# Optimization experiments

Measured on AMD Instinct MI355X. Metric: run time of the kernel, lower is better.

The kernel has to match this reference:

```python
import jax, jax.numpy as jnp
import numpy as np
from jax import lax

SEQ, BATCH, IN, H, L = 2048, 64, 512, 3, 4


def setup_inputs() -> dict:
    key = jax.random.key(0)
    ks = jax.random.split(key, 10)
    s_in = 1.0 / np.sqrt(H)  # torch GRU init scale: U(-1/sqrt(H), 1/sqrt(H))
    u = lambda k, shape: jax.random.uniform(k, shape, jnp.float32, -s_in, s_in)
    return {
        "x": jax.random.normal(ks[0], (SEQ, BATCH, IN), jnp.float32),
        "hxs": jnp.zeros((L, BATCH, H), jnp.float32),
        "w_ih0": u(ks[1], (3 * H, IN)),
        "w_hh0": u(ks[2], (3 * H, H)),
        "b_ih0": u(ks[3], (3 * H,)),
        "b_hh0": u(ks[4], (3 * H,)),
        "w_ih_rest": u(ks[5], (L - 1, 3 * H, H)),
        "w_hh_rest": u(ks[6], (L - 1, 3 * H, H)),
        "b_ih_rest": u(ks[7], (L - 1, 3 * H)),
        "b_hh_rest": u(ks[8], (L - 1, 3 * H)),
    }


def _gru_layer(x_seq, h0, w_ih, w_hh, b_ih, b_hh):
    # Precompute input projections for the whole sequence: (T, B, 3H)
    gx = jnp.einsum("tbi,gi->tbg", x_seq, w_ih) + b_ih

    def step(h, gx_t):
        gh = h @ w_hh.T + b_hh  # (B, 3H)
        rx, zx, nx = jnp.split(gx_t, 3, axis=-1)
        rh, zh, nh = jnp.split(gh, 3, axis=-1)
        r = jax.nn.sigmoid(rx + rh)
        z = jax.nn.sigmoid(zx + zh)
        n = jnp.tanh(nx + r * nh)
        h_new = (1.0 - z) * n + z * h
        return h_new, h_new

    h_last, ys = lax.scan(step, h0, gx)
    return ys, h_last


def reference(x, hxs, w_ih0, w_hh0, b_ih0, b_hh0, w_ih_rest, w_hh_rest, b_ih_rest, b_hh_rest):
    out, h = _gru_layer(x, hxs[0], w_ih0, w_hh0, b_ih0, b_hh0)
    h_finals = [h]
    for l in range(w_ih_rest.shape[0]):  # small fixed layer count
        out, h = _gru_layer(out, hxs[l + 1], w_ih_rest[l], w_hh_rest[l], b_ih_rest[l], b_hh_rest[l])
        h_finals.append(h)
    return out, jnp.stack(h_finals)  # (T, B, H), (L, B, H)
```

## Files before the change

### kernel.cpp

```cpp
#include <hip/hip_runtime.h>
#include <hip/hip_bf16.h>

#define T_SEQ 2048
#define CHUNK 16
#define NCHUNK 129
#define L2E  1.44269504088896340736f
#define L2E2 2.88539008177792681472f

typedef float vf2 __attribute__((ext_vector_type(2)));

template<int CTRL>
__device__ __forceinline__ float dppmov(float v) {
    return __int_as_float(__builtin_amdgcn_update_dpp(
        0, __float_as_int(v), CTRL, 0xF, 0xF, true));
}
template<int CTRL>
__device__ __forceinline__ float dppadd(float v) { return v + dppmov<CTRL>(v); }
__device__ __forceinline__ float swzadd16(float v) {
    return v + __int_as_float(__builtin_amdgcn_ds_swizzle(__float_as_int(v), 0x401F));
}
__device__ __forceinline__ float frcp(float x) { return __builtin_amdgcn_rcpf(x); }
__device__ __forceinline__ float ex2(float x)  { return __builtin_amdgcn_exp2f(x); }
__device__ __forceinline__ vf2 pkfma(vf2 a, float b, vf2 c) {
    vf2 bb = { b, b };
    return __builtin_elementwise_fma(a, bb, c);
}

#define RING_BARRIER() asm volatile("s_waitcnt lgkmcnt(0)\ns_barrier" ::: "memory")

__global__ __launch_bounds__(256) void gx0_kernel(
    const float* __restrict__ x, const float* __restrict__ w,
    const float* __restrict__ bias, float* __restrict__ gx0)
{
    const int lane = threadIdx.x & 63;
    const int gw   = (blockIdx.x * 256 + threadIdx.x) >> 6;

    float4 wA[9], wB[9];
#pragma unroll
    for (int g = 0; g < 9; ++g) {
        const float s = (g < 6) ? L2E : -L2E2;
        float4 a = *(const float4*)&w[g * 512 + lane * 4];
        float4 b = *(const float4*)&w[g * 512 + 256 + lane * 4];
        wA[g] = make_float4(a.x * s, a.y * s, a.z * s, a.w * s);
        wB[g] = make_float4(b.x * s, b.y * s, b.z * s, b.w * s);
    }
    const float bval = (lane < 9) ? bias[lane] * ((lane < 6) ? L2E : -L2E2) : 0.f;

    size_t row0 = (size_t)gw * 16;
    const float4* xp = (const float4*)(x + row0 * 512);
    float4 xa = xp[lane];
    float4 xb = xp[64 + lane];

#pragma unroll 1
    for (int i = 0; i < 16; ++i) {
        float4 na = xa, nb = xb;
        if (i < 15) {
            na = xp[(i + 1) * 128 + lane];
            nb = xp[(i + 1) * 128 + 64 + lane];
        }
        float r[9];
#pragma unroll
        for (int g = 0; g < 9; ++g) {
            float s = xa.x * wA[g].x;
            s = fmaf(xa.y, wA[g].y, s);
            s = fmaf(xa.z, wA[g].z, s);
            s = fmaf(xa.w, wA[g].w, s);
            s = fmaf(xb.x, wB[g].x, s);
            s = fmaf(xb.y, wB[g].y, s);
            s = fmaf(xb.z, wB[g].z, s);
            s = fmaf(xb.w, wB[g].w, s);
            s = dppadd<0xB1>(s);
            s = dppadd<0x4E>(s);
            s = dppadd<0x124>(s);
            s = dppadd<0x128>(s);
            s = swzadd16(s);
            s += __shfl_xor(s, 32, 64);
            r[g] = s;
        }
        float o = r[0];
#pragma unroll
        for (int g = 1; g < 9; ++g) o = (lane == g) ? r[g] : o;
        if (lane < 9) gx0[(row0 + i) * 9 + lane] = fminf(fmaxf(o + bval, -50.f), 50.f);
        xa = na; xb = nb;
    }
}

__global__ __launch_bounds__(128) void gru_scan(
    const float* __restrict__ gx0,
    const float* __restrict__ hxs,
    const float* __restrict__ w_hh0, const float* __restrict__ b_hh0,
    const float* __restrict__ w_ih_rest, const float* __restrict__ w_hh_rest,
    const float* __restrict__ b_ih_rest, const float* __restrict__ b_hh_rest,
    float* __restrict__ out)
{
    __shared__ float gxf[3 * CHUNK * 3 * 64];
    __shared__ float ring[2][CHUNK][64];
    const int tid  = threadIdx.x;
    const int lane = tid & 63;

    if (tid < 64) {
        __builtin_amdgcn_s_setprio(1);
        const int grp = lane >> 4;
        const int r_  = lane & 15;
        const int l   = r_ >> 2;
        const int j   = r_ & 3;
        const bool jok = (j < 3);
        const bool is0 = (l == 0);
        const int  b   = blockIdx.x * 4 + grp;
        const int  row0 = jok ? j : 0;

        int lx[4];
#pragma unroll
        for (int q = 0; q < 4; ++q) lx[q] = lane ^ (q << 2);

        vf2 wi01[3], wh01[3], bh01;
        float wi2[3], wh2[3], bh2;
        {
            float wi[3][3], wh[3][3], bh[3];
            const float sc[3] = {L2E, L2E, -L2E2};
#pragma unroll
            for (int m = 0; m < 3; ++m) {
                const int row = m * 3 + row0;
                if (l == 0) {
                    bh[m] = b_hh0[row] * sc[m];
#pragma unroll
                    for (int k = 0; k < 3; ++k) { wi[m][k] = 0.f; wh[m][k] = w_hh0[row * 3 + k] * sc[m]; }
                } else {
                    float bb = b_hh_rest[(l - 1) * 9 + row];
                    if (m < 2) bb += b_ih_rest[(l - 1) * 9 + row];
                    bh[m] = bb * sc[m];
#pragma unroll
                    for (int k = 0; k < 3; ++k) {
                        wi[m][k] = w_ih_rest[((l - 1) * 9 + row) * 3 + k] * sc[m];
                        wh[m][k] = w_hh_rest[((l - 1) * 9 + row) * 3 + k] * sc[m];
                    }
                }
            }
#pragma unroll
            for (int k = 0; k < 3; ++k) {
                wi01[k] = (vf2){wi[0][k], wi[1][k]};
                wh01[k] = (vf2){wh[0][k], wh[1][k]};
                wi2[k] = wi[2][k]; wh2[k] = wh[2][k];
            }
            bh01 = (vf2){bh[0], bh[1]};
            bh2  = bh[2];
        }
        const float bi2 = is0 ? 0.f : b_ih_rest[(l - 1) * 9 + 6 + row0] * (-L2E2);

        if (!(is0 && jok)) {
            const float cm[3] = {0.f, 0.f, bi2};
#pragma unroll
            for (int f = 0; f < 3; ++f)
                for (int st = 0; st < CHUNK; ++st)
#pragma unroll
                    for (int m = 0; m < 3; ++m)
                        gxf[((f * CHUNK + st) * 3 + m) * 64 + lx[(st * 3 + m) & 3]] = cm[m];
        }
        float h = jok ? hxs[(l * 64 + b) * 3 + j] : 0.f;

        RING_BARRIER();

        float gp[4][3];
#define PREF(SL, BUF, ST)                                                           \
        do {                                                                        \
            const float* _r = gxf + ((BUF) * CHUNK + (ST)) * 192;                   \
            gp[SL][0] = _r[lx[((ST) * 3 + 0) & 3]];                                 \
            gp[SL][1] = _r[64 + lx[((ST) * 3 + 1) & 3]];                            \
            gp[SL][2] = _r[128 + lx[((ST) * 3 + 2) & 3]];                           \
        } while (0)

#pragma unroll
        for (int k = 0; k < 4; ++k) PREF(k, 0, k);

        int bufc = 0;

#define GSTEP(P, MODE, TT)                                                          \
        do {                                                                        \
            float c0 = gp[(P) & 3][0], c1 = gp[(P) & 3][1], c2 = gp[(P) & 3][2];    \
            if ((P) < CHUNK - 4) PREF((P) & 3, bufc, (P) + 4);                      \
            else                 PREF((P) & 3, bufn, (P) - (CHUNK - 4));            \
            float hv0 = dppmov<0x00>(h);                                            \
            float hv1 = dppmov<0x55>(h);                                            \
            float hv2 = dppmov<0xAA>(h);                                            \
            float xv0 = dppmov<0x114>(hv0);                                         \
            float xv1 = dppmov<0x114>(hv1);                                         \
            float xv2 = dppmov<0x114>(hv2);                                         \
            vf2 t1 = pkfma(wh01[0], hv0, bh01);                                     \
            vf2 t2 = pkfma(wh01[1], hv1, (vf2){c0, c1});                            \
            t1 = pkfma(wh01[2], hv2, t1);                                           \
            t2 = pkfma(wi01[0], xv0, t2);                                           \
            t1 = pkfma(wi01[1], xv1, t1);                                           \
            t2 = pkfma(wi01[2], xv2, t2);                                           \
            vf2 arz = t1 + t2;                                                      \
            float ghn = fmaf(wh2[0], hv0, fmaf(wh2[1], hv1, fmaf(wh2[2], hv2, bh2))); \
            float gxn = fmaf(wi2[0], xv0, fmaf(wi2[1], xv1, fmaf(wi2[2], xv2, c2))); \
            float er = ex2(-arz.x);                                                 \
            float ez = ex2(-arz.y);                                                 \
            float rr = frcp(1.0f + er);                                             \
            float argn = fmaf(rr, ghn, gxn);                                        \
            float en = ex2(argn);                                                   \
            float hm = h - ez;                                                      \
            float hp = h + ez;                                                      \
            float N  = fmaf(en, hm, hp);                                            \
            float enp1 = en + 1.0f;                                                 \
            float D  = fmaf(enp1, ez, enp1);                                        \
            float hn = N * frcp(D);                                                 \
            if (MODE == 0)      h = ((TT) >= 0)    ? hn : h;                        \
            else if (MODE == 2) h = ((TT) < T_SEQ) ? hn : h;                        \
            else                h = hn;                                             \
            ring[CB][(P)][lane] = hn;                                               \
        } while (0)

        {
            const int bufn = 1; const int CB = 0;
#pragma unroll
            for (int p = 0; p < 4; ++p)  GSTEP(p, 0, p - l);
#pragma unroll
            for (int p = 4; p < 16; ++p) GSTEP(p, 1, 0);
            RING_BARRIER();
            bufc = 1;
        }
#pragma unroll 1
        for (int c = 1; c < 128; ++c) {
            const int bufn = (bufc == 2) ? 0 : bufc + 1;
            const int CB = c & 1;
#pragma unroll
            for (int p = 0; p < 16; ++p) GSTEP(p, 1, 0);
            RING_BARRIER();
            bufc = bufn;
        }
        {
            const int bufn = (bufc == 2) ? 0 : bufc + 1;
            const int CB = 0;
#pragma unroll
            for (int p = 0; p < 4; ++p) GSTEP(p, 2, 2048 + p - l);
            RING_BARRIER();
        }
#undef GSTEP
#undef PREF
        if (jok) out[(size_t)T_SEQ * 192 + (l * 64 + b) * 3 + j] = h;
    } else {
        const int blk = blockIdx.x;

#define FILL(F, T0)                                                                 \
        do {                                                                        \
            _Pragma("unroll")                                                       \
            for (int k = 0; k < 9; ++k) {                                           \
                int i   = k * 64 + lane;                                            \
                int st  = i / 36;                                                   \
                int rem = i - st * 36;                                              \
                int m   = rem / 12;                                                 \
                int pos = rem - m * 12;                                             \
                int bl  = pos / 3;                                                  \
                int jj  = pos - bl * 3;                                             \
                float val = gx0[(size_t)((T0) + st) * 576 + (blk * 4 + bl) * 9 + m * 3 + jj]; \
                int slot = (bl * 16 + jj) ^ ((((st * 3 + m) & 3)) << 2);            \
                gxf[(((F) * CHUNK + st) * 3 + m) * 64 + slot] = val;                \
            }                                                                       \
        } while (0)

#define DRAIN(CC)                                                                   \
        do {                                                                        \
            _Pragma("unroll")                                                       \
            for (int k = 0; k < 3; ++k) {                                           \
                int i  = k * 64 + lane;                                             \
                int p  = i / 12;                                                    \
                int q  = i - p * 12;                                                \
                int g2 = q / 3;                                                     \
                int jj = q - g2 * 3;                                                \
                int t  = (CC) * CHUNK + p - 3;                                      \
                float val = ring[(CC) & 1][p][g2 * 16 + 12 + jj];                   \
                if (t >= 0 && t < T_SEQ)                                            \
                    out[(size_t)t * 192 + (blk * 4 + g2) * 3 + jj] = val;           \
            }                                                                       \
        } while (0)

        FILL(0, 0);
        FILL(1, CHUNK);
        RING_BARRIER();

#pragma unroll 1
        for (int c = 0; c < NCHUNK; ++c) {
            const int f = c + 2;
            if (f <= 127) FILL(f % 3, f * CHUNK);
            if (c >= 1)   DRAIN(c - 1);
            RING_BARRIER();
        }
        DRAIN(NCHUNK - 1);
#undef FILL
#undef DRAIN
    }
}

extern "C" void kernel_launch(void* const* d_in, const int* in_sizes, int n_in,
                              void* d_out, int out_size, void* d_ws, size_t ws_size,
                              hipStream_t stream) {
    const float* x         = (const float*)d_in[0];
    const float* hxs       = (const float*)d_in[1];
    const float* w_ih0     = (const float*)d_in[2];
    const float* w_hh0     = (const float*)d_in[3];
    const float* b_ih0     = (const float*)d_in[4];
    const float* b_hh0     = (const float*)d_in[5];
    const float* w_ih_rest = (const float*)d_in[6];
    const float* w_hh_rest = (const float*)d_in[7];
    const float* b_ih_rest = (const float*)d_in[8];
    const float* b_hh_rest = (const float*)d_in[9];
    float* out = (float*)d_out;
    float* gx0 = (float*)d_ws;

    hipLaunchKernelGGL(gx0_kernel, dim3(2048), dim3(256), 0, stream,
                       x, w_ih0, b_ih0, gx0);
    hipLaunchKernelGGL(gru_scan, dim3(16), dim3(128), 0, stream,
                       gx0, hxs, w_hh0, b_hh0, w_ih_rest, w_hh_rest,
                       b_ih_rest, b_hh_rest, out);
}
```

Measured before the change: 227.3 us.

## Merge producer wave into compute wave, removing per-chunk block barriers

The scan kernel drops the separate loader/drainer wavefront and runs with a single 64-lane wave that prefetches gx0 chunks into registers, commits them to padded shared memory after each chunk, and writes outputs directly to global memory from the last-layer lanes. This removes the s_barrier synchronisation between two waves every chunk and the ring buffer for outputs. The cost is that global loads and stores now sit in the latency-critical recurrence wave, and the shared layout changes from an XOR swizzle to a 68-float padded stride.

After: 269.4 us. 18.5% more time.

```diff
diff --git a/kernel.cpp b/kernel.cpp
--- a/kernel.cpp
+++ b/kernel.cpp
@@ -3,7 +3,6 @@
 
 #define T_SEQ 2048
 #define CHUNK 16
-#define NCHUNK 129
 #define L2E  1.44269504088896340736f
 #define L2E2 2.88539008177792681472f
 
@@ -25,8 +24,6 @@
     vf2 bb = { b, b };
     return __builtin_elementwise_fma(a, bb, c);
 }
-
-#define RING_BARRIER() asm volatile("s_waitcnt lgkmcnt(0)\ns_barrier" ::: "memory")
 
 __global__ __launch_bounds__(256) void gx0_kernel(
     const float* __restrict__ x, const float* __restrict__ w,
@@ -85,7 +82,7 @@
     }
 }
 
-__global__ __launch_bounds__(128) void gru_scan(
+__global__ __launch_bounds__(64) void gru_scan(
     const float* __restrict__ gx0,
     const float* __restrict__ hxs,
     const float* __restrict__ w_hh0, const float* __restrict__ b_hh0,
@@ -93,203 +90,181 @@
     const float* __restrict__ b_ih_rest, const float* __restrict__ b_hh_rest,
     float* __restrict__ out)
 {
-    __shared__ float gxf[3 * CHUNK * 3 * 64];
-    __shared__ float ring[2][CHUNK][64];
-    const int tid  = threadIdx.x;
-    const int lane = tid & 63;
-
-    if (tid < 64) {
-        __builtin_amdgcn_s_setprio(1);
-        const int grp = lane >> 4;
-        const int r_  = lane & 15;
-        const int l   = r_ >> 2;
-        const int j   = r_ & 3;
-        const bool jok = (j < 3);
-        const bool is0 = (l == 0);
-        const int  b   = blockIdx.x * 4 + grp;
-        const int  row0 = jok ? j : 0;
-
-        int lx[4];
-#pragma unroll
-        for (int q = 0; q < 4; ++q) lx[q] = lane ^ (q << 2);
-
-        vf2 wi01[3], wh01[3], bh01;
-        float wi2[3], wh2[3], bh2;
-        {
-            float wi[3][3], wh[3][3], bh[3];
-            const float sc[3] = {L2E, L2E, -L2E2};
-#pragma unroll
-            for (int m = 0; m < 3; ++m) {
-                const int row = m * 3 + row0;
-                if (l == 0) {
-                    bh[m] = b_hh0[row] * sc[m];
-#pragma unroll
-                    for (int k = 0; k < 3; ++k) { wi[m][k] = 0.f; wh[m][k] = w_hh0[row * 3 + k] * sc[m]; }
-                } else {
-                    float bb = b_hh_rest[(l - 1) * 9 + row];
-                    if (m < 2) bb += b_ih_rest[(l - 1) * 9 + row];
-                    bh[m] = bb * sc[m];
-#pragma unroll
-                    for (int k = 0; k < 3; ++k) {
-                        wi[m][k] = w_ih_rest[((l - 1) * 9 + row) * 3 + k] * sc[m];
-                        wh[m][k] = w_hh_rest[((l - 1) * 9 + row) * 3 + k] * sc[m];
-                    }
+    __shared__ float gxf[3 * CHUNK * 3 * 68];
+    const int lane = threadIdx.x;
+    const int grp  = lane >> 4;
+    const int r_   = lane & 15;
+    const int l    = r_ >> 2;
+    const int j    = r_ & 3;
+    const bool jok = (j < 3);
+    const bool is0 = (l == 0);
+    const bool do_store = (l == 3) && jok;
+    const int  b   = blockIdx.x * 4 + grp;
+    const int  row0 = jok ? j : 0;
+
+    vf2 wi01[3], wh01[3], bh01;
+    float wi2[3], wh2[3], bh2;
+    {
+        float wi[3][3], wh[3][3], bh[3];
+        const float sc[3] = {L2E, L2E, -L2E2};
+#pragma unroll
+        for (int m = 0; m < 3; ++m) {
+            const int row = m * 3 + row0;
+            if (l == 0) {
+                bh[m] = b_hh0[row] * sc[m];
+#pragma unroll
+                for (int k = 0; k < 3; ++k) { wi[m][k] = 0.f; wh[m][k] = w_hh0[row * 3 + k] * sc[m]; }
+            } else {
+                float bb = b_hh_rest[(l - 1) * 9 + row];
+                if (m < 2) bb += b_ih_rest[(l - 1) * 9 + row];
+                bh[m] = bb * sc[m];
+#pragma unroll
+                for (int k = 0; k < 3; ++k) {
+                    wi[m][k] = w_ih_rest[((l - 1) * 9 + row) * 3 + k] * sc[m];
+                    wh[m][k] = w_hh_rest[((l - 1) * 9 + row) * 3 + k] * sc[m];
                 }
             }
-#pragma unroll
-            for (int k = 0; k < 3; ++k) {
-                wi01[k] = (vf2){wi[0][k], wi[1][k]};
-                wh01[k] = (vf2){wh[0][k], wh[1][k]};
-                wi2[k] = wi[2][k]; wh2[k] = wh[2][k];
-            }
-            bh01 = (vf2){bh[0], bh[1]};
-            bh2  = bh[2];
-        }
-        const float bi2 = is0 ? 0.f : b_ih_rest[(l - 1) * 9 + 6 + row0] * (-L2E2);
-
-        if (!(is0 && jok)) {
-            const float cm[3] = {0.f, 0.f, bi2};
-#pragma unroll
-            for (int f = 0; f < 3; ++f)
-                for (int st = 0; st < CHUNK; ++st)
-#pragma unroll
-                    for (int m = 0; m < 3; ++m)
-                        gxf[((f * CHUNK + st) * 3 + m) * 64 + lx[(st * 3 + m) & 3]] = cm[m];
-        }
-        float h = jok ? hxs[(l * 64 + b) * 3 + j] : 0.f;
-
-        RING_BARRIER();
-
-        float gp[4][3];
+        }
+#pragma unroll
+        for (int k = 0; k < 3; ++k) {
+            wi01[k] = (vf2){wi[0][k], wi[1][k]};
+            wh01[k] = (vf2){wh[0][k], wh[1][k]};
+            wi2[k] = wi[2][k]; wh2[k] = wh[2][k];
+        }
+        bh01 = (vf2){bh[0], bh[1]};
+        bh2  = bh[2];
+    }
+    const float bi2 = is0 ? 0.f : b_ih_rest[(l - 1) * 9 + 6 + row0] * (-L2E2);
+
+    if (!(is0 && jok)) {
+        const float cm[3] = {0.f, 0.f, bi2};
+#pragma unroll
+        for (int f = 0; f < 3; ++f)
+            for (int st = 0; st < CHUNK; ++st)
+#pragma unroll
+                for (int m = 0; m < 3; ++m)
+                    gxf[((f * CHUNK + st) * 3 + m) * 68 + lane] = cm[m];
+    }
+    float h = jok ? hxs[(l * 64 + b) * 3 + j] : 0.f;
+
+    int goff[9], loff[9];
+#pragma unroll
+    for (int k = 0; k < 9; ++k) {
+        int i   = k * 64 + lane;
+        int st  = i / 36;
+        int rem = i - st * 36;
+        int m   = rem / 12;
+        int pos = rem - m * 12;
+        int bl  = pos / 3;
+        int jj  = pos - bl * 3;
+        goff[k] = st * 576 + ((int)blockIdx.x * 4 + bl) * 9 + m * 3 + jj;
+        loff[k] = (st * 3 + m) * 68 + bl * 16 + jj;
+    }
+
+    float fv[9];
+#define FLOAD(C)                                                                    \
+    do { const float* _g = gx0 + (size_t)(C) * (CHUNK * 576);                       \
+         _Pragma("unroll") for (int k = 0; k < 9; ++k) fv[k] = _g[goff[k]]; } while (0)
+#define FCOMMIT(F)                                                                  \
+    do { _Pragma("unroll") for (int k = 0; k < 9; ++k)                              \
+             gxf[(F) * (CHUNK * 204) + loff[k]] = fv[k]; } while (0)
+
+    FLOAD(0); FCOMMIT(0);
+    FLOAD(1); FCOMMIT(1);
+    asm volatile("s_waitcnt lgkmcnt(0)" ::: "memory");
+
+    float gp[4][3];
 #define PREF(SL, BUF, ST)                                                           \
-        do {                                                                        \
-            const float* _r = gxf + ((BUF) * CHUNK + (ST)) * 192;                   \
-            gp[SL][0] = _r[lx[((ST) * 3 + 0) & 3]];                                 \
-            gp[SL][1] = _r[64 + lx[((ST) * 3 + 1) & 3]];                            \
-            gp[SL][2] = _r[128 + lx[((ST) * 3 + 2) & 3]];                           \
-        } while (0)
-
-#pragma unroll
-        for (int k = 0; k < 4; ++k) PREF(k, 0, k);
-
-        int bufc = 0;
+    do { const float* _r = gxf + ((BUF) * CHUNK + (ST)) * 204 + lane;               \
+         gp[SL][0] = _r[0]; gp[SL][1] = _r[68]; gp[SL][2] = _r[136]; } while (0)
+
+#pragma unroll
+    for (int k = 0; k < 4; ++k) PREF(k, 0, k);
+
+    int soff = -3 * 192 + b * 3 + j;
 
 #define GSTEP(P, MODE, TT)                                                          \
-        do {                                                                        \
-            float c0 = gp[(P) & 3][0], c1 = gp[(P) & 3][1], c2 = gp[(P) & 3][2];    \
-            if ((P) < CHUNK - 4) PREF((P) & 3, bufc, (P) + 4);                      \
-            else                 PREF((P) & 3, bufn, (P) - (CHUNK - 4));            \
-            float hv0 = dppmov<0x00>(h);                                            \
-            float hv1 = dppmov<0x55>(h);                                            \
-            float hv2 = dppmov<0xAA>(h);                                            \
-            float xv0 = dppmov<0x114>(hv0);                                         \
-            float xv1 = dppmov<0x114>(hv1);                                         \
-            float xv2 = dppmov<0x114>(hv2);                                         \
-            vf2 t1 = pkfma(wh01[0], hv0, bh01);                                     \
-            vf2 t2 = pkfma(wh01[1], hv1, (vf2){c0, c1});                            \
-            t1 = pkfma(wh01[2], hv2, t1);                                           \
-            t2 = pkfma(wi01[0], xv0, t2);                                           \
-            t1 = pkfma(wi01[1], xv1, t1);                                           \
-            t2 = pkfma(wi01[2], xv2, t2);                                           \
-            vf2 arz = t1 + t2;                                                      \
-            float ghn = fmaf(wh2[0], hv0, fmaf(wh2[1], hv1, fmaf(wh2[2], hv2, bh2))); \
-            float gxn = fmaf(wi2[0], xv0, fmaf(wi2[1], xv1, fmaf(wi2[2], xv2, c2))); \
-            float er = ex2(-arz.x);                                                 \
-            float ez = ex2(-arz.y);                                                 \
-            float rr = frcp(1.0f + er);                                             \
-            float argn = fmaf(rr, ghn, gxn);                                        \
-            float en = ex2(argn);                                                   \
-            float hm = h - ez;                                                      \
-            float hp = h + ez;                                                      \
-            float N  = fmaf(en, hm, hp);                                            \
-            float enp1 = en + 1.0f;                                                 \
-            float D  = fmaf(enp1, ez, enp1);                                        \
-            float hn = N * frcp(D);                                                 \
-            if (MODE == 0)      h = ((TT) >= 0)    ? hn : h;                        \
-            else if (MODE == 2) h = ((TT) < T_SEQ) ? hn : h;                        \
-            else                h = hn;                                             \
-            ring[CB][(P)][lane] = hn;                                               \
-        } while (0)
-
-        {
-            const int bufn = 1; const int CB = 0;
-#pragma unroll
-            for (int p = 0; p < 4; ++p)  GSTEP(p, 0, p - l);
-#pragma unroll
-            for (int p = 4; p < 16; ++p) GSTEP(p, 1, 0);
-            RING_BARRIER();
-            bufc = 1;
-        }
+    do {                                                                            \
+        float c0 = gp[(P) & 3][0], c1 = gp[(P) & 3][1], c2 = gp[(P) & 3][2];        \
+        if ((P) < CHUNK - 4) PREF((P) & 3, bufc, (P) + 4);                          \
+        else                 PREF((P) & 3, bufn, (P) - (CHUNK - 4));                \
+        float hv0 = dppmov<0x00>(h);                                                \
+        float hv1 = dppmov<0x55>(h);                                                \
+        float hv2 = dppmov<0xAA>(h);                                                \
+        float xv0 = dppmov<0x114>(hv0);                                             \
+        float xv1 = dppmov<0x114>(hv1);                                             \
+        float xv2 = dppmov<0x114>(hv2);                                             \
+        vf2 t1 = pkfma(wh01[0], hv0, bh01);                                         \
+        vf2 t2 = pkfma(wh01[1], hv1, (vf2){c0, c1});                                \
+        t1 = pkfma(wh01[2], hv2, t1);                                               \
+        t2 = pkfma(wi01[0], xv0, t2);                                               \
+        t1 = pkfma(wi01[1], xv1, t1);                                               \
+        t2 = pkfma(wi01[2], xv2, t2);                                               \
+        vf2 arz = t1 + t2;                                                          \
+        float ghn = fmaf(wh2[0], hv0, fmaf(wh2[1], hv1, fmaf(wh2[2], hv2, bh2)));   \
+        float gxn = fmaf(wi2[0], xv0, fmaf(wi2[1], xv1, fmaf(wi2[2], xv2, c2)));    \
+        float er = ex2(-arz.x);                                                     \
+        float ez = ex2(-arz.y);                                                     \
+        float rr = frcp(1.0f + er);                                                 \
+        float argn = fmaf(rr, ghn, gxn);                                            \
+        float en = ex2(argn);                                                       \
+        vf2 hmhp = (vf2){h, h} + (vf2){-ez, ez};                                    \
+        float N  = fmaf(en, hmhp.x, hmhp.y);                                        \
+        float enp1 = en + 1.0f;                                                     \
+        float D  = fmaf(enp1, ez, enp1);                                            \
+        float hn = N * frcp(D);                                                     \
+        bool act = true;                                                            \
+        if (MODE == 0)      act = ((TT) >= 0);                                      \
+        else if (MODE == 2) act = ((TT) < T_SEQ);                                   \
+        h = act ? hn : h;                                                           \
+        if (do_store && act) out[soff] = hn;                                        \
+        soff += 192;                                                                \
+    } while (0)
+
+    {
+        const int bufc = 0, bufn = 1;
+        FLOAD(2);
+#pragma unroll
+        for (int p = 0; p < 4; ++p)  GSTEP(p, 0, p - l);
+#pragma unroll
+        for (int p = 4; p < 16; ++p) GSTEP(p, 1, 0);
+        FCOMMIT(2);
+    }
 #pragma unroll 1
-        for (int c = 1; c < 128; ++c) {
-            const int bufn = (bufc == 2) ? 0 : bufc + 1;
-            const int CB = c & 1;
-#pragma unroll
-            for (int p = 0; p < 16; ++p) GSTEP(p, 1, 0);
-            RING_BARRIER();
-            bufc = bufn;
-        }
-        {
-            const int bufn = (bufc == 2) ? 0 : bufc + 1;
-            const int CB = 0;
-#pragma unroll
-            for (int p = 0; p < 4; ++p) GSTEP(p, 2, 2048 + p - l);
-            RING_BARRIER();
-        }
+    for (int c = 1; c <= 125; ++c) {
+        const int bufc = c % 3;
+        const int bufn = (c + 1) % 3;
+        const int buff = (c + 2) % 3;
+        FLOAD(c + 2);
+#pragma unroll
+        for (int p = 0; p < 16; ++p) GSTEP(p, 1, 0);
+        switch (buff) {
+            case 0: FCOMMIT(0); break;
+            case 1: FCOMMIT(1); break;
+            default: FCOMMIT(2); break;
+        }
+    }
+    {
+        const int bufc = 0, bufn = 1;
+#pragma unroll
+        for (int p = 0; p < 16; ++p) GSTEP(p, 1, 0);
+    }
+    {
+        const int bufc = 1, bufn = 2;
+#pragma unroll
+        for (int p = 0; p < 16; ++p) GSTEP(p, 1, 0);
+    }
+    {
+        const int bufc = 2, bufn = 0;
+#pragma unroll
+        for (int p = 0; p < 4; ++p) GSTEP(p, 2, 2048 + p - l);
+    }
 #undef GSTEP
 #undef PREF
-        if (jok) out[(size_t)T_SEQ * 192 + (l * 64 + b) * 3 + j] = h;
-    } else {
-        const int blk = blockIdx.x;
-
-#define FILL(F, T0)                                                                 \
-        do {                                                                        \
-            _Pragma("unroll")                                                       \
-            for (int k = 0; k < 9; ++k) {                                           \
-                int i   = k * 64 + lane;                                            \
-                int st  = i / 36;                                                   \
-                int rem = i - st * 36;                                              \
-                int m   = rem / 12;                                                 \
-                int pos = rem - m * 12;                                             \
-                int bl  = pos / 3;                                                  \
-                int jj  = pos - bl * 3;                                             \
-                float val = gx0[(size_t)((T0) + st) * 576 + (blk * 4 + bl) * 9 + m * 3 + jj]; \
-                int slot = (bl * 16 + jj) ^ ((((st * 3 + m) & 3)) << 2);            \
-                gxf[(((F) * CHUNK + st) * 3 + m) * 64 + slot] = val;                \
-            }                                                                       \
-        } while (0)
-
-#define DRAIN(CC)                                                                   \
-        do {                                                                        \
-            _Pragma("unroll")                                                       \
-            for (int k = 0; k < 3; ++k) {                                           \
-                int i  = k * 64 + lane;                                             \
-                int p  = i / 12;                                                    \
-                int q  = i - p * 12;                                                \
-                int g2 = q / 3;                                                     \
-                int jj = q - g2 * 3;                                                \
-                int t  = (CC) * CHUNK + p - 3;                                      \
-                float val = ring[(CC) & 1][p][g2 * 16 + 12 + jj];                   \
-                if (t >= 0 && t < T_SEQ)                                            \
-                    out[(size_t)t * 192 + (blk * 4 + g2) * 3 + jj] = val;           \
-            }                                                                       \
-        } while (0)
-
-        FILL(0, 0);
-        FILL(1, CHUNK);
-        RING_BARRIER();
-
-#pragma unroll 1
-        for (int c = 0; c < NCHUNK; ++c) {
-            const int f = c + 2;
-            if (f <= 127) FILL(f % 3, f * CHUNK);
-            if (c >= 1)   DRAIN(c - 1);
-            RING_BARRIER();
-        }
-        DRAIN(NCHUNK - 1);
-#undef FILL
-#undef DRAIN
-    }
+#undef FLOAD
+#undef FCOMMIT
+
+    if (jok) out[(size_t)T_SEQ * 192 + (l * 64 + b) * 3 + j] = h;
 }
 
 extern "C" void kernel_launch(void* const* d_in, const int* in_sizes, int n_in,
@@ -310,7 +285,7 @@
 
     hipLaunchKernelGGL(gx0_kernel, dim3(2048), dim3(256), 0, stream,
                        x, w_ih0, b_ih0, gx0);
-    hipLaunchKernelGGL(gru_scan, dim3(16), dim3(128), 0, stream,
+    hipLaunchKernelGGL(gru_scan, dim3(16), dim3(64), 0, stream,
                        gx0, hxs, w_hh0, b_hh0, w_ih_rest, w_hh_rest,
                        b_ih_rest, b_hh_rest, out);
 }
```

## Fuse input projection and GRU scan into one kernel with per-chunk flag sync

Applied to the files above, without the earlier changes.

Merges the gx0 projection kernel and the recurrent scan into a single launch. Blocks with index 16 and up compute projections and bump a per-chunk atomic counter, while the 16 scan blocks spin on those counters before filling each chunk. The intent is to overlap the projection with the sequential scan and remove the second launch. It also swaps the XOR-swizzled LDS layout for a padded stride of 68, and adds a memset plus spin-waits that depend on the projection blocks being scheduled alongside the scan blocks.

Result: slower. 583.9 us (+156.8%).

```diff
diff --git a/kernel.cpp b/kernel.cpp
--- a/kernel.cpp
+++ b/kernel.cpp
@@ -4,8 +4,10 @@
 #define T_SEQ 2048
 #define CHUNK 16
 #define NCHUNK 129
+#define NSCAN 16
 #define L2E  1.44269504088896340736f
 #define L2E2 2.88539008177792681472f
+#define GX0_FLOATS (T_SEQ * 64 * 9)
 
 typedef float vf2 __attribute__((ext_vector_type(2)));
 
@@ -28,75 +30,85 @@
 
 #define RING_BARRIER() asm volatile("s_waitcnt lgkmcnt(0)\ns_barrier" ::: "memory")
 
-__global__ __launch_bounds__(256) void gx0_kernel(
-    const float* __restrict__ x, const float* __restrict__ w,
-    const float* __restrict__ bias, float* __restrict__ gx0)
+__global__ __launch_bounds__(128) void fused_gru(
+    const float* __restrict__ x,
+    const float* __restrict__ hxs,
+    const float* __restrict__ w_ih0, const float* __restrict__ w_hh0,
+    const float* __restrict__ b_ih0, const float* __restrict__ b_hh0,
+    const float* __restrict__ w_ih_rest, const float* __restrict__ w_hh_rest,
+    const float* __restrict__ b_ih_rest, const float* __restrict__ b_hh_rest,
+    float* __restrict__ out,
+    float* __restrict__ gx0,
+    int*   __restrict__ cnt)
 {
     const int lane = threadIdx.x & 63;
-    const int gw   = (blockIdx.x * 256 + threadIdx.x) >> 6;
-
-    float4 wA[9], wB[9];
-#pragma unroll
-    for (int g = 0; g < 9; ++g) {
-        const float s = (g < 6) ? L2E : -L2E2;
-        float4 a = *(const float4*)&w[g * 512 + lane * 4];
-        float4 b = *(const float4*)&w[g * 512 + 256 + lane * 4];
-        wA[g] = make_float4(a.x * s, a.y * s, a.z * s, a.w * s);
-        wB[g] = make_float4(b.x * s, b.y * s, b.z * s, b.w * s);
+
+    if (blockIdx.x >= NSCAN) {
+        const int wid = threadIdx.x >> 6;
+        const int gw  = ((int)blockIdx.x - NSCAN) * 2 + wid;
+
+        float4 wA[9], wB[9];
+#pragma unroll
+        for (int g = 0; g < 9; ++g) {
+            const float s = (g < 6) ? L2E : -L2E2;
+            float4 a = *(const float4*)&w_ih0[g * 512 + lane * 4];
+            float4 b = *(const float4*)&w_ih0[g * 512 + 256 + lane * 4];
+            wA[g] = make_float4(a.x * s, a.y * s, a.z * s, a.w * s);
+            wB[g] = make_float4(b.x * s, b.y * s, b.z * s, b.w * s);
+        }
+        const float bval = (lane < 9) ? b_ih0[lane] * ((lane < 6) ? L2E : -L2E2) : 0.f;
+
+        size_t row0 = (size_t)gw * 16;
+        const float4* xp = (const float4*)(x + row0 * 512);
+        float4 xa = xp[lane];
+        float4 xb = xp[64 + lane];
+
+#pragma unroll 1
+        for (int i = 0; i < 16; ++i) {
+            float4 na = xa, nb = xb;
+            if (i < 15) {
+                na = xp[(i + 1) * 128 + lane];
+                nb = xp[(i + 1) * 128 + 64 + lane];
+            }
+            float r[9];
+#pragma unroll
+            for (int g = 0; g < 9; ++g) {
+                float s = xa.x * wA[g].x;
+                s = fmaf(xa.y, wA[g].y, s);
+                s = fmaf(xa.z, wA[g].z, s);
+                s = fmaf(xa.w, wA[g].w, s);
+                s = fmaf(xb.x, wB[g].x, s);
+                s = fmaf(xb.y, wB[g].y, s);
+                s = fmaf(xb.z, wB[g].z, s);
+                s = fmaf(xb.w, wB[g].w, s);
+                s = dppadd<0xB1>(s);
+                s = dppadd<0x4E>(s);
+                s = dppadd<0x124>(s);
+                s = dppadd<0x128>(s);
+                s = swzadd16(s);
+                s += __shfl_xor(s, 32, 64);
+                r[g] = s;
+            }
+            float o = r[0];
+#pragma unroll
+            for (int g = 1; g < 9; ++g) o = (lane == g) ? r[g] : o;
+            if (lane < 9) {
+                float v = fminf(fmaxf(o + bval, -50.f), 50.f);
+                __hip_atomic_store((unsigned int*)(gx0 + (row0 + i) * 9 + lane),
+                                   __float_as_uint(v),
+                                   __ATOMIC_RELAXED, __HIP_MEMORY_SCOPE_AGENT);
+            }
+            xa = na; xb = nb;
+        }
+        if (lane == 0)
+            __hip_atomic_fetch_add(&cnt[gw >> 6], 1,
+                                   __ATOMIC_RELEASE, __HIP_MEMORY_SCOPE_AGENT);
+        return;
     }
-    const float bval = (lane < 9) ? bias[lane] * ((lane < 6) ? L2E : -L2E2) : 0.f;
-
-    size_t row0 = (size_t)gw * 16;
-    const float4* xp = (const float4*)(x + row0 * 512);
-    float4 xa = xp[lane];
-    float4 xb = xp[64 + lane];
-
-#pragma unroll 1
-    for (int i = 0; i < 16; ++i) {
-        float4 na = xa, nb = xb;
-        if (i < 15) {
-            na = xp[(i + 1) * 128 + lane];
-            nb = xp[(i + 1) * 128 + 64 + lane];
-        }
-        float r[9];
-#pragma unroll
-        for (int g = 0; g < 9; ++g) {
-            float s = xa.x * wA[g].x;
-            s = fmaf(xa.y, wA[g].y, s);
-            s = fmaf(xa.z, wA[g].z, s);
-            s = fmaf(xa.w, wA[g].w, s);
-            s = fmaf(xb.x, wB[g].x, s);
-            s = fmaf(xb.y, wB[g].y, s);
-            s = fmaf(xb.z, wB[g].z, s);
-            s = fmaf(xb.w, wB[g].w, s);
-            s = dppadd<0xB1>(s);
-            s = dppadd<0x4E>(s);
-            s = dppadd<0x124>(s);
-            s = dppadd<0x128>(s);
-            s = swzadd16(s);
-            s += __shfl_xor(s, 32, 64);
-            r[g] = s;
-        }
-        float o = r[0];
-#pragma unroll
-        for (int g = 1; g < 9; ++g) o = (lane == g) ? r[g] : o;
-        if (lane < 9) gx0[(row0 + i) * 9 + lane] = fminf(fmaxf(o + bval, -50.f), 50.f);
-        xa = na; xb = nb;
-    }
-}
-
-__global__ __launch_bounds__(128) void gru_scan(
-    const float* __restrict__ gx0,
-    const float* __restrict__ hxs,
-    const float* __restrict__ w_hh0, const float* __restrict__ b_hh0,
-    const float* __restrict__ w_ih_rest, const float* __restrict__ w_hh_rest,
-    const float* __restrict__ b_ih_rest, const float* __restrict__ b_hh_rest,
-    float* __restrict__ out)
-{
-    __shared__ float gxf[3 * CHUNK * 3 * 64];
+
+    __shared__ float gxf[3 * CHUNK * 3 * 68];
     __shared__ float ring[2][CHUNK][64];
-    const int tid  = threadIdx.x;
-    const int lane = tid & 63;
+    const int tid = threadIdx.x;
 
     if (tid < 64) {
         __builtin_amdgcn_s_setprio(1);
@@ -109,10 +121,6 @@
         const int  b   = blockIdx.x * 4 + grp;
         const int  row0 = jok ? j : 0;
 
-        int lx[4];
-#pragma unroll
-        for (int q = 0; q < 4; ++q) lx[q] = lane ^ (q << 2);
-
         vf2 wi01[3], wh01[3], bh01;
         float wi2[3], wh2[3], bh2;
         {
@@ -154,7 +162,7 @@
                 for (int st = 0; st < CHUNK; ++st)
 #pragma unroll
                     for (int m = 0; m < 3; ++m)
-                        gxf[((f * CHUNK + st) * 3 + m) * 64 + lx[(st * 3 + m) & 3]] = cm[m];
+                        gxf[((f * CHUNK + st) * 3 + m) * 68 + lane] = cm[m];
         }
         float h = jok ? hxs[(l * 64 + b) * 3 + j] : 0.f;
 
@@ -162,12 +170,8 @@
 
         float gp[4][3];
 #define PREF(SL, BUF, ST)                                                           \
-        do {                                                                        \
-            const float* _r = gxf + ((BUF) * CHUNK + (ST)) * 192;                   \
-            gp[SL][0] = _r[lx[((ST) * 3 + 0) & 3]];                                 \
-            gp[SL][1] = _r[64 + lx[((ST) * 3 + 1) & 3]];                            \
-            gp[SL][2] = _r[128 + lx[((ST) * 3 + 2) & 3]];                           \
-        } while (0)
+        do { const float* _r = gxf + ((BUF) * CHUNK + (ST)) * 204 + lane;           \
+             gp[SL][0] = _r[0]; gp[SL][1] = _r[68]; gp[SL][2] = _r[136]; } while (0)
 
 #pragma unroll
         for (int k = 0; k < 4; ++k) PREF(k, 0, k);
@@ -199,9 +203,8 @@
             float rr = frcp(1.0f + er);                                             \
             float argn = fmaf(rr, ghn, gxn);                                        \
             float en = ex2(argn);                                                   \
-            float hm = h - ez;                                                      \
-            float hp = h + ez;                                                      \
-            float N  = fmaf(en, hm, hp);                                            \
+            vf2 hmhp = (vf2){h, h} + (vf2){-ez, ez};                                \
+            float N  = fmaf(en, hmhp.x, hmhp.y);                                    \
             float enp1 = en + 1.0f;                                                 \
             float D  = fmaf(enp1, ez, enp1);                                        \
             float hn = N * frcp(D);                                                 \
@@ -241,6 +244,11 @@
         if (jok) out[(size_t)T_SEQ * 192 + (l * 64 + b) * 3 + j] = h;
     } else {
         const int blk = blockIdx.x;
+
+#define WAITCHUNK(TC)                                                               \
+        do { while (__hip_atomic_load(&cnt[TC], __ATOMIC_ACQUIRE,                   \
+                                      __HIP_MEMORY_SCOPE_AGENT) < 64)               \
+                 __builtin_amdgcn_s_sleep(8); } while (0)
 
 #define FILL(F, T0)                                                                 \
         do {                                                                        \
@@ -253,9 +261,12 @@
                 int pos = rem - m * 12;                                             \
                 int bl  = pos / 3;                                                  \
                 int jj  = pos - bl * 3;                                             \
-                float val = gx0[(size_t)((T0) + st) * 576 + (blk * 4 + bl) * 9 + m * 3 + jj]; \
-                int slot = (bl * 16 + jj) ^ ((((st * 3 + m) & 3)) << 2);            \
-                gxf[(((F) * CHUNK + st) * 3 + m) * 64 + slot] = val;                \
+                unsigned int raw = __hip_atomic_load(                               \
+                    (const unsigned int*)(gx0 + (size_t)((T0) + st) * 576           \
+                                          + (blk * 4 + bl) * 9 + m * 3 + jj),       \
+                    __ATOMIC_RELAXED, __HIP_MEMORY_SCOPE_AGENT);                    \
+                gxf[((F) * CHUNK + st) * 204 + m * 68 + bl * 16 + jj]               \
+                    = __uint_as_float(raw);                                         \
             }                                                                       \
         } while (0)
 
@@ -275,20 +286,28 @@
             }                                                                       \
         } while (0)
 
-        FILL(0, 0);
-        FILL(1, CHUNK);
+        WAITCHUNK(0); FILL(0, 0);
+        WAITCHUNK(1); FILL(1, CHUNK);
         RING_BARRIER();
 
 #pragma unroll 1
         for (int c = 0; c < NCHUNK; ++c) {
             const int f = c + 2;
-            if (f <= 127) FILL(f % 3, f * CHUNK);
-            if (c >= 1)   DRAIN(c - 1);
+            if (f <= 127) {
+                WAITCHUNK(f);
+                switch (f % 3) {
+                    case 0: FILL(0, f * CHUNK); break;
+                    case 1: FILL(1, f * CHUNK); break;
+                    default: FILL(2, f * CHUNK); break;
+                }
+            }
+            if (c >= 1) DRAIN(c - 1);
             RING_BARRIER();
         }
         DRAIN(NCHUNK - 1);
 #undef FILL
 #undef DRAIN
+#undef WAITCHUNK
     }
 }
 
@@ -307,10 +326,11 @@
     const float* b_hh_rest = (const float*)d_in[9];
     float* out = (float*)d_out;
     float* gx0 = (float*)d_ws;
-
-    hipLaunchKernelGGL(gx0_kernel, dim3(2048), dim3(256), 0, stream,
-                       x, w_ih0, b_ih0, gx0);
-    hipLaunchKernelGGL(gru_scan, dim3(16), dim3(128), 0, stream,
-                       gx0, hxs, w_hh0, b_hh0, w_ih_rest, w_hh_rest,
-                       b_ih_rest, b_hh_rest, out);
-}
+    int*   cnt = (int*)((char*)d_ws + (size_t)GX0_FLOATS * 4);
+
+    hipMemsetAsync(cnt, 0, 128 * sizeof(int), stream);
+    hipLaunchKernelGGL(fused_gru, dim3(NSCAN + 4096), dim3(128), 0, stream,
+                       x, hxs, w_ih0, w_hh0, b_ih0, b_hh0,
+                       w_ih_rest, w_hh_rest, b_ih_rest, b_hh_rest,
+                       out, gx0, cnt);
+}
```
